# Performance work log

Hardware: AMD Instinct MI355X
Metric: run time of the kernel (lower is better)

The kernel has to match this reference:

```python
import jax, jax.numpy as jnp
from jax import lax
import numpy as np

H = 32  # hidden_size

def setup_inputs() -> dict:
    key = jax.random.key(0)
    ks = jax.random.split(key, 7)
    B, T = 32, 16384
    s = 1.0 / np.sqrt(H)  # torch LSTM/Linear init scale
    x = jax.random.normal(ks[0], (B, T, 1), dtype=jnp.float32)
    W_ih = jax.random.uniform(ks[1], (4 * H, 1), jnp.float32, -s, s)
    W_hh = jax.random.uniform(ks[2], (4 * H, H), jnp.float32, -s, s)
    b_ih = jax.random.uniform(ks[3], (4 * H,), jnp.float32, -s, s)
    b_hh = jax.random.uniform(ks[4], (4 * H,), jnp.float32, -s, s)
    W_out = jax.random.uniform(ks[5], (1, H), jnp.float32, -s, s)
    b_out = jax.random.uniform(ks[6], (1,), jnp.float32, -s, s)
    return {"x": x, "W_ih": W_ih, "W_hh": W_hh, "b_ih": b_ih,
            "b_hh": b_hh, "W_out": W_out, "b_out": b_out}

def reference(x, W_ih, W_hh, b_ih, b_hh, W_out, b_out):
    B, T, _ = x.shape
    # Precompute input contribution to all gates once: (B, T, 4H)
    pre = jnp.einsum('bti,gi->btg', x, W_ih) + b_ih + b_hh

    def step(carry, p_t):
        h, c = carry
        gates = p_t + h @ W_hh.T  # (B, 4H), torch gate order i,f,g,o
        i, f, g, o = jnp.split(gates, 4, axis=-1)
        c = jax.nn.sigmoid(f) * c + jax.nn.sigmoid(i) * jnp.tanh(g)
        h = jax.nn.sigmoid(o) * jnp.tanh(c)
        return (h, c), h

    h0 = jnp.zeros((B, H), x.dtype)
    (_, _), hs = lax.scan(step, (h0, h0), jnp.swapaxes(pre, 0, 1))
    hs = jnp.swapaxes(hs, 0, 1)  # (B, T, H)
    return hs @ W_out.T + b_out  # (B, T, 1)
```

## Files before the change

### kernel.cpp

```cpp
#include <hip/hip_runtime.h>

#define T_LEN 16384
#define BATCH 32
#define HID 32
#define L2E 1.44269504088896340736f

typedef float f2 __attribute__((ext_vector_type(2)));

#if __has_builtin(__builtin_amdgcn_exp2f)
#define EXP2F(x) __builtin_amdgcn_exp2f(x)
#else
#define EXP2F(x) __exp2f(x)
#endif
#if __has_builtin(__builtin_amdgcn_rcpf)
#define RCPF(x) __builtin_amdgcn_rcpf(x)
#else
#define RCPF(x) (1.0f / (x))
#endif

__device__ __forceinline__ float rlane(float v, int lane) {
    return __int_as_float(__builtin_amdgcn_readlane(__float_as_int(v), lane));
}

__device__ __forceinline__ float xhalf_lo_to_hi(float v) {
#if __has_builtin(__builtin_amdgcn_permlane32_swap)
    typedef unsigned u2_t __attribute__((ext_vector_type(2)));
    u2_t r = __builtin_amdgcn_permlane32_swap(__float_as_uint(v), __float_as_uint(v),
                                              false, false);
    return __uint_as_float(r.x);
#else
    return __shfl_xor(v, 32, 64);
#endif
}

__global__ __launch_bounds__(64) __attribute__((amdgpu_waves_per_eu(1, 1)))
void lstm_seq_kernel(const float* __restrict__ x,
                     const float* __restrict__ W_ih,
                     const float* __restrict__ W_hh,
                     const float* __restrict__ b_ih,
                     const float* __restrict__ b_hh,
                     const float* __restrict__ W_out,
                     const float* __restrict__ b_out,
                     float* __restrict__ out)
{
    const int b    = blockIdx.x;
    const int lane = threadIdx.x;
    const int j    = lane & 31;
    const bool upper = (lane >= 32);

    const int rowA = upper ? (32 + j) : j;
    const int rowB = upper ? (96 + j) : (64 + j);

    f2 Wa2[16], Wb2[16];
    const f2* ra2 = reinterpret_cast<const f2*>(W_hh + (size_t)rowA * HID);
    const f2* rb2 = reinterpret_cast<const f2*>(W_hh + (size_t)rowB * HID);
    #pragma unroll
    for (int q = 0; q < 16; ++q) { Wa2[q] = ra2[q]; Wb2[q] = rb2[q]; }
    #pragma unroll
    for (int q = 0; q < 16; ++q) { asm("" : "+v"(Wa2[q]), "+v"(Wb2[q])); }

    const float wihA = W_ih[rowA];
    const float wihB = W_ih[rowB];
    const float bA = b_ih[rowA] + b_hh[rowA];
    const float bB = b_ih[rowB] + b_hh[rowB];

    const float sB = upper ? L2E : (2.0f * L2E);
    const float mB = upper ? 1.0f : 2.0f;
    const float aB = upper ? 0.0f : -1.0f;

    const float wout = W_out[j];
    const float bout = b_out[0];

    __shared__ float phist[64 * 65];
    __shared__ float hbuf[64];

    float c = 0.0f, h = 0.0f;
    hbuf[lane] = 0.0f;
    __syncthreads();

    const float* xb = x + (size_t)b * T_LEN;
    float*       yb = out + (size_t)b * T_LEN;
    const f2* hb2 = reinterpret_cast<const f2*>(&hbuf[32]);

    float xv = xb[lane];

    for (int t0 = 0; t0 < T_LEN; t0 += 64) {
        float xv_next = (t0 + 64 < T_LEN) ? xb[t0 + 64 + lane] : 0.0f;

        #pragma unroll 4
        for (int s = 0; s < 64; ++s) {
            const float xs  = rlane(xv, s);
            const float xpA = fmaf(xs, wihA, bA);
            const float xpB = fmaf(xs, wihB, bB);

            f2 hv2[16];
            #pragma unroll
            for (int p = 0; p < 16; ++p) hv2[p] = hb2[p];

            f2 zA[4], zB[4];
            #pragma unroll
            for (int p = 0; p < 16; ++p) {
                if (p < 4) {
                    asm("v_pk_mul_f32 %0, %1, %2"
                        : "=v"(zA[p]) : "v"(hv2[p]), "v"(Wa2[p]));
                    asm("v_pk_mul_f32 %0, %1, %2"
                        : "=v"(zB[p]) : "v"(hv2[p]), "v"(Wb2[p]));
                } else {
                    asm("v_pk_fma_f32 %0, %1, %2, %0"
                        : "+v"(zA[p & 3]) : "v"(hv2[p]), "v"(Wa2[p]));
                    asm("v_pk_fma_f32 %0, %1, %2, %0"
                        : "+v"(zB[p & 3]) : "v"(hv2[p]), "v"(Wb2[p]));
                }
            }
            const f2 rA = (zA[0] + zA[1]) + (zA[2] + zA[3]);
            const f2 rB = (zB[0] + zB[1]) + (zB[2] + zB[3]);
            const float za = (rA.x + rA.y) + xpA;
            const float zb = (rB.x + rB.y) + xpB;

            const float A  = RCPF(1.0f + EXP2F(-za * L2E));
            const float r  = RCPF(1.0f + EXP2F(-zb * sB));
            const float Bv = fmaf(r, mB, aB);

            const float u  = A * Bv;
            const float tu = xhalf_lo_to_hi(u);

            c = fmaf(A, c, tu);
            const float th = fmaf(2.0f, RCPF(1.0f + EXP2F(-2.0f * L2E * c)), -1.0f);
            h = Bv * th;

            hbuf[lane] = h;
            phist[s * 65 + lane] = h * wout;
        }

        __syncthreads();
        float acc = bout;
        #pragma unroll
        for (int k = 0; k < HID; ++k) acc += phist[lane * 65 + 32 + k];
        yb[t0 + lane] = acc;
        __syncthreads();

        xv = xv_next;
    }
}

extern "C" void kernel_launch(void* const* d_in, const int* in_sizes, int n_in,
                              void* d_out, int out_size, void* d_ws, size_t ws_size,
                              hipStream_t stream) {
    const float* x     = (const float*)d_in[0];
    const float* W_ih  = (const float*)d_in[1];
    const float* W_hh  = (const float*)d_in[2];
    const float* b_ih  = (const float*)d_in[3];
    const float* b_hh  = (const float*)d_in[4];
    const float* W_out = (const float*)d_in[5];
    const float* b_out = (const float*)d_in[6];
    float* out = (float*)d_out;

    lstm_seq_kernel<<<BATCH, 64, 0, stream>>>(x, W_ih, W_hh, b_ih, b_hh,
                                              W_out, b_out, out);
}
```

Baseline: 3.182 ms.

## Split hidden dot product across wave halves, computing all four gates per lane

Each lane now computes all four gate pre-activations for one hidden unit over half the hidden dimension, and the halves are combined with a cross-half permlane sum. The log2e sigmoid/tanh scaling is folded into the recurrent and input weights, and per-step LDS reads of h are halved. This shortens the dependent FMA chain and removes per-lane branches on gate type, in exchange for four cross-lane exchanges and more transcendental ops per step.

Result: slower. 3.727 ms (+17.1%).

```diff
diff --git a/kernel.cpp b/kernel.cpp
--- a/kernel.cpp
+++ b/kernel.cpp
@@ -6,6 +6,7 @@
 #define L2E 1.44269504088896340736f
 
 typedef float f2 __attribute__((ext_vector_type(2)));
+typedef unsigned u2_t __attribute__((ext_vector_type(2)));
 
 #if __has_builtin(__builtin_amdgcn_exp2f)
 #define EXP2F(x) __builtin_amdgcn_exp2f(x)
@@ -22,14 +23,13 @@
     return __int_as_float(__builtin_amdgcn_readlane(__float_as_int(v), lane));
 }
 
-__device__ __forceinline__ float xhalf_lo_to_hi(float v) {
+__device__ __forceinline__ float xhalf_sum(float v) {
 #if __has_builtin(__builtin_amdgcn_permlane32_swap)
-    typedef unsigned u2_t __attribute__((ext_vector_type(2)));
     u2_t r = __builtin_amdgcn_permlane32_swap(__float_as_uint(v), __float_as_uint(v),
                                               false, false);
-    return __uint_as_float(r.x);
+    return __uint_as_float(r.x) + __uint_as_float(r.y);
 #else
-    return __shfl_xor(v, 32, 64);
+    return v + __shfl_xor(v, 32, 64);
 #endif
 }
 
@@ -46,27 +46,38 @@
     const int b    = blockIdx.x;
     const int lane = threadIdx.x;
     const int j    = lane & 31;
-    const bool upper = (lane >= 32);
+    const int kbase = (lane & 32) >> 1;
 
-    const int rowA = upper ? (32 + j) : j;
-    const int rowB = upper ? (96 + j) : (64 + j);
+    const float sclS = -L2E;
+    const float sclG = -2.0f * L2E;
 
-    f2 Wa2[16], Wb2[16];
-    const f2* ra2 = reinterpret_cast<const f2*>(W_hh + (size_t)rowA * HID);
-    const f2* rb2 = reinterpret_cast<const f2*>(W_hh + (size_t)rowB * HID);
+    f2 Wi2[8], Wf2[8], Wg2[8], Wo2[8];
+    {
+        const f2* ri = (const f2*)(W_hh + (size_t)(     j) * HID + kbase);
+        const f2* rf = (const f2*)(W_hh + (size_t)(32 + j) * HID + kbase);
+        const f2* rg = (const f2*)(W_hh + (size_t)(64 + j) * HID + kbase);
+        const f2* ro = (const f2*)(W_hh + (size_t)(96 + j) * HID + kbase);
+        #pragma unroll
+        for (int p = 0; p < 8; ++p) {
+            Wi2[p] = ri[p] * sclS;
+            Wf2[p] = rf[p] * sclS;
+            Wg2[p] = rg[p] * sclG;
+            Wo2[p] = ro[p] * sclS;
+        }
+    }
     #pragma unroll
-    for (int q = 0; q < 16; ++q) { Wa2[q] = ra2[q]; Wb2[q] = rb2[q]; }
-    #pragma unroll
-    for (int q = 0; q < 16; ++q) { asm("" : "+v"(Wa2[q]), "+v"(Wb2[q])); }
+    for (int p = 0; p < 8; ++p) {
+        asm("" : "+v"(Wi2[p]), "+v"(Wf2[p]), "+v"(Wg2[p]), "+v"(Wo2[p]));
+    }
 
-    const float wihA = W_ih[rowA];
-    const float wihB = W_ih[rowB];
-    const float bA = b_ih[rowA] + b_hh[rowA];
-    const float bB = b_ih[rowB] + b_hh[rowB];
-
-    const float sB = upper ? L2E : (2.0f * L2E);
-    const float mB = upper ? 1.0f : 2.0f;
-    const float aB = upper ? 0.0f : -1.0f;
+    const float wih_i = 0.5f * sclS * W_ih[j];
+    const float wih_f = 0.5f * sclS * W_ih[32 + j];
+    const float wih_g = 0.5f * sclG * W_ih[64 + j];
+    const float wih_o = 0.5f * sclS * W_ih[96 + j];
+    const float bi = 0.5f * sclS * (b_ih[     j] + b_hh[     j]);
+    const float bf = 0.5f * sclS * (b_ih[32 + j] + b_hh[32 + j]);
+    const float bg = 0.5f * sclG * (b_ih[64 + j] + b_hh[64 + j]);
+    const float bo = 0.5f * sclS * (b_ih[96 + j] + b_hh[96 + j]);
 
     const float wout = W_out[j];
     const float bout = b_out[0];
@@ -78,55 +89,66 @@
     hbuf[lane] = 0.0f;
     __syncthreads();
 
-    const float* xb = x + (size_t)b * T_LEN;
-    float*       yb = out + (size_t)b * T_LEN;
-    const f2* hb2 = reinterpret_cast<const f2*>(&hbuf[32]);
+    const float* xb_ptr = x + (size_t)b * T_LEN;
+    float*       yb     = out + (size_t)b * T_LEN;
+    const f2* hb2 = reinterpret_cast<const f2*>(&hbuf[kbase]);
 
-    float xv = xb[lane];
+    float xv = xb_ptr[lane];
 
     for (int t0 = 0; t0 < T_LEN; t0 += 64) {
-        float xv_next = (t0 + 64 < T_LEN) ? xb[t0 + 64 + lane] : 0.0f;
+        float xv_next = (t0 + 64 < T_LEN) ? xb_ptr[t0 + 64 + lane] : 0.0f;
 
         #pragma unroll 4
         for (int s = 0; s < 64; ++s) {
             const float xs  = rlane(xv, s);
-            const float xpA = fmaf(xs, wihA, bA);
-            const float xpB = fmaf(xs, wihB, bB);
+            const float xbi = fmaf(xs, wih_i, bi);
+            const float xbf = fmaf(xs, wih_f, bf);
+            const float xbg = fmaf(xs, wih_g, bg);
+            const float xbo = fmaf(xs, wih_o, bo);
 
-            f2 hv2[16];
+            f2 hv2[8];
             #pragma unroll
-            for (int p = 0; p < 16; ++p) hv2[p] = hb2[p];
+            for (int p = 0; p < 8; ++p) hv2[p] = hb2[p];
 
-            f2 zA[4], zB[4];
+            f2 ai0, ai1, af0, af1, ag0, ag1, ao0, ao1;
+            asm("v_pk_mul_f32 %0, %1, %2" : "=v"(ai0) : "v"(hv2[0]), "v"(Wi2[0]));
+            asm("v_pk_mul_f32 %0, %1, %2" : "=v"(ai1) : "v"(hv2[1]), "v"(Wi2[1]));
+            asm("v_pk_mul_f32 %0, %1, %2" : "=v"(af0) : "v"(hv2[0]), "v"(Wf2[0]));
+            asm("v_pk_mul_f32 %0, %1, %2" : "=v"(af1) : "v"(hv2[1]), "v"(Wf2[1]));
+            asm("v_pk_mul_f32 %0, %1, %2" : "=v"(ag0) : "v"(hv2[0]), "v"(Wg2[0]));
+            asm("v_pk_mul_f32 %0, %1, %2" : "=v"(ag1) : "v"(hv2[1]), "v"(Wg2[1]));
+            asm("v_pk_mul_f32 %0, %1, %2" : "=v"(ao0) : "v"(hv2[0]), "v"(Wo2[0]));
+            asm("v_pk_mul_f32 %0, %1, %2" : "=v"(ao1) : "v"(hv2[1]), "v"(Wo2[1]));
             #pragma unroll
-            for (int p = 0; p < 16; ++p) {
-                if (p < 4) {
-                    asm("v_pk_mul_f32 %0, %1, %2"
-                        : "=v"(zA[p]) : "v"(hv2[p]), "v"(Wa2[p]));
-                    asm("v_pk_mul_f32 %0, %1, %2"
-                        : "=v"(zB[p]) : "v"(hv2[p]), "v"(Wb2[p]));
-                } else {
-                    asm("v_pk_fma_f32 %0, %1, %2, %0"
-                        : "+v"(zA[p & 3]) : "v"(hv2[p]), "v"(Wa2[p]));
-                    asm("v_pk_fma_f32 %0, %1, %2, %0"
-                        : "+v"(zB[p & 3]) : "v"(hv2[p]), "v"(Wb2[p]));
-                }
+            for (int p = 2; p < 8; p += 2) {
+                asm("v_pk_fma_f32 %0, %1, %2, %0" : "+v"(ai0) : "v"(hv2[p  ]), "v"(Wi2[p  ]));
+                asm("v_pk_fma_f32 %0, %1, %2, %0" : "+v"(ai1) : "v"(hv2[p+1]), "v"(Wi2[p+1]));
+                asm("v_pk_fma_f32 %0, %1, %2, %0" : "+v"(af0) : "v"(hv2[p  ]), "v"(Wf2[p  ]));
+                asm("v_pk_fma_f32 %0, %1, %2, %0" : "+v"(af1) : "v"(hv2[p+1]), "v"(Wf2[p+1]));
+                asm("v_pk_fma_f32 %0, %1, %2, %0" : "+v"(ag0) : "v"(hv2[p  ]), "v"(Wg2[p  ]));
+                asm("v_pk_fma_f32 %0, %1, %2, %0" : "+v"(ag1) : "v"(hv2[p+1]), "v"(Wg2[p+1]));
+                asm("v_pk_fma_f32 %0, %1, %2, %0" : "+v"(ao0) : "v"(hv2[p  ]), "v"(Wo2[p  ]));
+                asm("v_pk_fma_f32 %0, %1, %2, %0" : "+v"(ao1) : "v"(hv2[p+1]), "v"(Wo2[p+1]));
             }
-            const f2 rA = (zA[0] + zA[1]) + (zA[2] + zA[3]);
-            const f2 rB = (zB[0] + zB[1]) + (zB[2] + zB[3]);
-            const float za = (rA.x + rA.y) + xpA;
-            const float zb = (rB.x + rB.y) + xpB;
+            const f2 Pi = ai0 + ai1, Pf = af0 + af1, Pg = ag0 + ag1, Po = ao0 + ao1;
+            const float pi = Pi.x + Pi.y + xbi;
+            const float pf = Pf.x + Pf.y + xbf;
+            const float pg = Pg.x + Pg.y + xbg;
+            const float po = Po.x + Po.y + xbo;
 
-            const float A  = RCPF(1.0f + EXP2F(-za * L2E));
-            const float r  = RCPF(1.0f + EXP2F(-zb * sB));
-            const float Bv = fmaf(r, mB, aB);
+            const float zi = xhalf_sum(pi);
+            const float zf = xhalf_sum(pf);
+            const float zg = xhalf_sum(pg);
+            const float zo = xhalf_sum(po);
 
-            const float u  = A * Bv;
-            const float tu = xhalf_lo_to_hi(u);
+            const float si = RCPF(1.0f + EXP2F(zi));
+            const float sf = RCPF(1.0f + EXP2F(zf));
+            const float tg = fmaf(2.0f, RCPF(1.0f + EXP2F(zg)), -1.0f);
+            const float so = RCPF(1.0f + EXP2F(zo));
 
-            c = fmaf(A, c, tu);
-            const float th = fmaf(2.0f, RCPF(1.0f + EXP2F(-2.0f * L2E * c)), -1.0f);
-            h = Bv * th;
+            c = fmaf(sf, c, si * tg);
+            const float th = fmaf(2.0f, RCPF(1.0f + EXP2F(sclG * c)), -1.0f);
+            h = so * th;
 
             hbuf[lane] = h;
             phist[s * 65 + lane] = h * wout;
@@ -135,7 +157,7 @@
         __syncthreads();
         float acc = bout;
         #pragma unroll
-        for (int k = 0; k < HID; ++k) acc += phist[lane * 65 + 32 + k];
+        for (int k = 0; k < HID; ++k) acc += phist[lane * 65 + k];
         yb[t0 + lane] = acc;
         __syncthreads();
 
```
